# Kernel tuning notes

Hardware: AMD Instinct MI355X
Metric: run time of the kernel (lower is better)

The kernel has to match this reference:

```python
import jax, jax.numpy as jnp
import numpy as np

B, N, F_IN, K, NUM_CLASSES = 16, 2048, 8, 35, 4
EPS = 1e-5


def _bn(x, g, b):
    # BatchNorm in training mode: stats over all leading (batch/node/edge) dims.
    ax = tuple(range(x.ndim - 1))
    mu = jnp.mean(x, axis=ax, keepdims=True)
    var = jnp.var(x, axis=ax, keepdims=True)
    return g * (x - mu) * jax.lax.rsqrt(var + EPS) + b


def _edge_feats(h, k):
    # h: [B,N,C]. Dynamic kNN within each graph (self included, as torch_cluster.knn),
    # then EdgeConv features cat([x_i, x_j - x_i]) -> [B,N,k,2C].
    sq = jnp.sum(h * h, -1)                                   # [B,N]
    d = sq[:, :, None] + sq[:, None, :] - 2.0 * jnp.einsum('bnc,bmc->bnm', h, h)
    _, idx = jax.lax.top_k(-d, k)                             # [B,N,k]
    hj = jax.vmap(lambda hb, ib: hb[ib])(h, idx)              # [B,N,k,C]
    hi = jnp.broadcast_to(h[:, :, None, :], hj.shape)
    return jnp.concatenate([hi, hj - hi], axis=-1)


def _forward(x, w1, b1, g1, bt1, w2, b2, g2, bt2, w3, b3, w4, b4,
             w5, b5, w6, b6, g6, bt6, w7, b7, g7, bt7, w8, b8):
    # conv1: DynamicEdgeConv(MLP([16,64,64,64]), k, 'max'); plain_last => 3rd linear bare
    e = _edge_feats(x, K)                                     # [B,N,K,16]
    h = jax.nn.relu(_bn(e @ w1 + b1, g1, bt1))
    h = jax.nn.relu(_bn(h @ w2 + b2, g2, bt2))
    h = h @ w3 + b3
    x1 = jnp.max(h, axis=2)                                   # [B,N,64] scatter-max over k
    # conv2: DynamicEdgeConv(MLP([128,128]), k, 'max'); single plain linear
    e2 = _edge_feats(x1, K)                                   # [B,N,K,128]
    x2 = jnp.max(e2 @ w4 + b4, axis=2)                        # [B,N,128]
    out = jnp.concatenate([x1, x2], axis=-1) @ w5 + b5        # [B,N,256]
    pooled = jnp.max(out, axis=1)                             # [B,256] global_max_pool
    # head MLP([256,128,64,4], dropout eval-mode, batch_norm), plain_last
    h = jax.nn.relu(_bn(pooled @ w6 + b6, g6, bt6))
    h = jax.nn.relu(_bn(h @ w7 + b7, g7, bt7))
    return h @ w8 + b8                                        # [B,4]


def setup_inputs() -> dict:
    key = jax.random.key(0)
    ks = jax.random.split(key, 12)

    def lin(kk, fi, fo):
        k1, k2 = jax.random.split(kk)
        w = jax.random.normal(k1, (fi, fo), jnp.float32) / np.sqrt(fi).astype(np.float32)
        b = jax.random.normal(k2, (fo,), jnp.float32) * 0.01
        return w, b

    x = jax.random.normal(ks[0], (B, N, F_IN), jnp.float32)
    w1, b1 = lin(ks[1], 2 * F_IN, 64)
    w2, b2 = lin(ks[2], 64, 64)
    w3, b3 = lin(ks[3], 64, 64)
    w4, b4 = lin(ks[4], 2 * 64, 128)
    w5, b5 = lin(ks[5], 128 + 64, 256)
    w6, b6 = lin(ks[6], 256, 128)
    w7, b7 = lin(ks[7], 128, 64)
    w8, b8 = lin(ks[8], 64, NUM_CLASSES)
    ones, zeros = jnp.ones, jnp.zeros
    return {
        'x': x,
        'w1': w1, 'b1': b1, 'g1': ones(64), 'bt1': zeros(64),
        'w2': w2, 'b2': b2, 'g2': ones(64), 'bt2': zeros(64),
        'w3': w3, 'b3': b3,
        'w4': w4, 'b4': b4,
        'w5': w5, 'b5': b5,
        'w6': w6, 'b6': b6, 'g6': ones(128), 'bt6': zeros(128),
        'w7': w7, 'b7': b7, 'g7': ones(64), 'bt7': zeros(64),
        'w8': w8, 'b8': b8,
    }


def reference(x, w1, b1, g1, bt1, w2, b2, g2, bt2, w3, b3, w4, b4,
              w5, b5, w6, b6, g6, bt6, w7, b7, g7, bt7, w8, b8):
    return _forward(x, w1, b1, g1, bt1, w2, b2, g2, bt2, w3, b3, w4, b4,
                    w5, b5, w6, b6, g6, bt6, w7, b7, g7, bt7, w8, b8)
```

## Files before the change

### kernel.cpp

```cpp
#include <hip/hip_runtime.h>
#include <cfloat>
#include <cstdint>

constexpr int Bn   = 16;
constexpr int Nn   = 2048;
constexpr int Fin  = 8;
constexpr int Kn   = 35;
constexpr int NODES = Bn * Nn;
constexpr int EDG   = NODES * Kn;
constexpr int NSTATB = 1024;
constexpr float EPSV = 1e-5f;

typedef _Float16 f16;
typedef _Float16 f16x2 __attribute__((ext_vector_type(2)));

__device__ __forceinline__ unsigned enc_f(float f){
    unsigned u = __float_as_uint(f);
    return (u & 0x80000000u) ? ~u : (u | 0x80000000u);
}
__device__ __forceinline__ float dec_f(unsigned e){
    unsigned u = (e & 0x80000000u) ? (e ^ 0x80000000u) : ~e;
    return __uint_as_float(u);
}

template<int C>
__global__ __launch_bounds__(256) void sq_kernel(const float* __restrict__ h, float* __restrict__ sq){
    int i = blockIdx.x * 256 + threadIdx.x;
    if (i >= NODES) return;
    const float* p = h + (size_t)i * C;
    float s = 0.f;
#pragma unroll
    for (int c = 0; c < C; c++) s += p[c] * p[c];
    sq[i] = s;
}

template<int C>
__global__ __launch_bounds__(256) void knn_kernel(const float* __restrict__ h, const float* __restrict__ sq,
                                                  int* __restrict__ idxout){
    __shared__ float dist[4][Nn];
    __shared__ float hi4[4][C];
    __shared__ float sqi[4];
    __shared__ float statred[4][2][4];
    __shared__ unsigned long long keybuf[4][128];
    int t  = threadIdx.x;
    int b  = blockIdx.x >> 9;
    int i0 = (blockIdx.x & 511) * 4;
    int w  = t >> 6, lane = t & 63;

    for (int i = t; i < 4 * C; i += 256)
        hi4[i / C][i % C] = h[((size_t)(b * Nn) + i0 + i / C) * C + (i % C)];
    if (t < 4) sqi[t] = sq[b * Nn + i0 + t];
    __syncthreads();

    const float4* H0 = (const float4*)hi4[0];
    const float4* H1 = (const float4*)hi4[1];
    const float4* H2 = (const float4*)hi4[2];
    const float4* H3 = (const float4*)hi4[3];
    float ps0=0.f,ps1=0.f,ps2=0.f,ps3=0.f, pq0=0.f,pq1=0.f,pq2=0.f,pq3=0.f;
    for (int j = t; j < Nn; j += 256){
        const float4* hj = (const float4*)(h + ((size_t)(b * Nn) + j) * C);
        float d0 = 0.f, d1 = 0.f, d2 = 0.f, d3 = 0.f;
#pragma unroll 4
        for (int c4 = 0; c4 < C / 4; c4++){
            float4 v = hj[c4];
            float4 a0 = H0[c4], a1 = H1[c4], a2 = H2[c4], a3 = H3[c4];
            d0 += a0.x*v.x + a0.y*v.y + a0.z*v.z + a0.w*v.w;
            d1 += a1.x*v.x + a1.y*v.y + a1.z*v.z + a1.w*v.w;
            d2 += a2.x*v.x + a2.y*v.y + a2.z*v.z + a2.w*v.w;
            d3 += a3.x*v.x + a3.y*v.y + a3.z*v.z + a3.w*v.w;
        }
        float sj = sq[b * Nn + j];
        float D0 = sqi[0] + sj - 2.f*d0; dist[0][j] = D0; ps0 += D0; pq0 += D0*D0;
        float D1 = sqi[1] + sj - 2.f*d1; dist[1][j] = D1; ps1 += D1; pq1 += D1*D1;
        float D2 = sqi[2] + sj - 2.f*d2; dist[2][j] = D2; ps2 += D2; pq2 += D2*D2;
        float D3 = sqi[3] + sj - 2.f*d3; dist[3][j] = D3; ps3 += D3; pq3 += D3*D3;
    }
#pragma unroll
    for (int d = 1; d < 64; d <<= 1){
        ps0 += __shfl_xor(ps0, d); pq0 += __shfl_xor(pq0, d);
        ps1 += __shfl_xor(ps1, d); pq1 += __shfl_xor(pq1, d);
        ps2 += __shfl_xor(ps2, d); pq2 += __shfl_xor(pq2, d);
        ps3 += __shfl_xor(ps3, d); pq3 += __shfl_xor(pq3, d);
    }
    if (lane == 0){
        statred[0][0][w] = ps0; statred[0][1][w] = pq0;
        statred[1][0][w] = ps1; statred[1][1][w] = pq1;
        statred[2][0][w] = ps2; statred[2][1][w] = pq2;
        statred[3][0][w] = ps3; statred[3][1][w] = pq3;
    }
    __syncthreads();

    const float* dw = dist[w];
    float smu = statred[w][0][0] + statred[w][0][1] + statred[w][0][2] + statred[w][0][3];
    float sqq = statred[w][1][0] + statred[w][1][1] + statred[w][1][2] + statred[w][1][3];
    float mu = smu * (1.f / (float)Nn);
    float sg = sqrtf(fmaxf(sqq * (1.f / (float)Nn) - mu * mu, 0.f));

    float lo = mu - 8.f * sg;  int clo = 0;
    float hi = FLT_MAX;        int chi = Nn;

    {
        float PV[5] = { mu - 2.5f*sg, mu - 1.9f*sg, mu - 1.45f*sg, mu - 1.1f*sg, mu };
        int CC[5] = {0,0,0,0,0};
        for (int s8 = 0; s8 < 32; s8 += 8){
            float vv[8];
#pragma unroll
            for (int u = 0; u < 8; u++) vv[u] = dw[(s8 + u) * 64 + lane];
#pragma unroll
            for (int pi = 0; pi < 5; pi++){
                int c = 0;
#pragma unroll
                for (int u = 0; u < 8; u++) c += __popcll(__ballot(vv[u] < PV[pi]));
                CC[pi] += c;
            }
        }
#pragma unroll
        for (int pi = 0; pi < 5; pi++){
            if (CC[pi] >= Kn){ if (PV[pi] < hi){ hi = PV[pi]; chi = CC[pi]; } }
            else             { if (PV[pi] > lo){ lo = PV[pi]; clo = CC[pi]; } }
        }
    }

    for (int it = 0; it < 24 && chi > 128; it++){
        int den = (chi - clo) > 0 ? (chi - clo) : 1;
        float piv = (it & 1) ? 0.5f * (lo + hi)
                             : lo + (hi - lo) * ((float)(96 - clo) / (float)den);
        if (!(piv > lo && piv < hi)) piv = 0.5f * (lo + hi);
        if (!(piv > lo && piv < hi)) break;
        int c = 0;
        for (int s8 = 0; s8 < 32; s8 += 8){
            float vv[8];
#pragma unroll
            for (int u = 0; u < 8; u++) vv[u] = dw[(s8 + u) * 64 + lane];
#pragma unroll
            for (int u = 0; u < 8; u++) c += __popcll(__ballot(vv[u] < piv));
        }
        if (c >= Kn){ hi = piv; chi = c; } else { lo = piv; clo = c; }
    }

    size_t obase = ((size_t)(b * Nn) + i0 + w) * Kn;

    if (chi <= 128){
        keybuf[w][lane]      = ~0ull;
        keybuf[w][lane + 64] = ~0ull;
        unsigned long long me_lower = (1ull << lane) - 1ull;
        int boff = 0;
        for (int s8 = 0; s8 < 32; s8 += 8){
            float vv[8];
#pragma unroll
            for (int u = 0; u < 8; u++) vv[u] = dw[(s8 + u) * 64 + lane];
#pragma unroll
            for (int u = 0; u < 8; u++){
                bool cnd = vv[u] < hi;
                unsigned long long m = __ballot(cnd);
                if (cnd){
                    int o = boff + __popcll(m & me_lower);
                    keybuf[w][o] = (((unsigned long long)enc_f(vv[u])) << 16) | (unsigned)((s8 + u) * 64 + lane);
                }
                boff += __popcll(m);
            }
        }
        unsigned long long k0 = keybuf[w][lane];
        unsigned long long k1 = keybuf[w][lane + 64];
        int r0 = 0, r1 = 0;
        int nR = (chi + 7) & ~7;
        for (int j2 = 0; j2 < nR; j2 += 8){
            unsigned long long a0 = keybuf[w][j2+0], a1 = keybuf[w][j2+1];
            unsigned long long a2 = keybuf[w][j2+2], a3 = keybuf[w][j2+3];
            unsigned long long a4 = keybuf[w][j2+4], a5 = keybuf[w][j2+5];
            unsigned long long a6 = keybuf[w][j2+6], a7 = keybuf[w][j2+7];
            r0 += (a0<k0)+(a1<k0)+(a2<k0)+(a3<k0)+(a4<k0)+(a5<k0)+(a6<k0)+(a7<k0);
            r1 += (a0<k1)+(a1<k1)+(a2<k1)+(a3<k1)+(a4<k1)+(a5<k1)+(a6<k1)+(a7<k1);
        }
        if (lane < chi      && r0 < Kn) idxout[obase + r0] = (int)(k0 & 0xffffu);
        if (lane + 64 < chi && r1 < Kn) idxout[obase + r1] = (int)(k1 & 0xffffu);
    } else {
        unsigned selmask = 0u;
        for (int e = 0; e < Kn; e++){
            unsigned long long best = ~0ull;
#pragma unroll
            for (int s = 0; s < 32; s++){
                float v = dw[s * 64 + lane];
                if (v < hi && !((selmask >> s) & 1)){
                    unsigned long long key = (((unsigned long long)enc_f(v)) << 16) | (unsigned)(s * 64 + lane);
                    best = (key < best) ? key : best;
                }
            }
#pragma unroll
            for (int d = 1; d < 64; d <<= 1){
                unsigned long long ov = __shfl_xor(best, d);
                best = (ov < best) ? ov : best;
            }
            int jj = (int)(best & 0xffffu);
            if ((jj & 63) == lane) selmask |= 1u << (jj >> 6);
            if (lane == 0) idxout[obase + e] = jj;
        }
    }
}

__global__ __launch_bounds__(256) void pre1_kernel(const float* __restrict__ x,
        const float* __restrict__ w1, const float* __restrict__ b1,
        float* __restrict__ p, float* __restrict__ q){
    int t = threadIdx.x, w = t >> 6, c = t & 63;
    float wd[8], wb[8];
#pragma unroll
    for (int f = 0; f < 8; f++){
        float wbv = w1[(8 + f) * 64 + c];
        wb[f] = wbv;
        wd[f] = w1[f * 64 + c] - wbv;
    }
    float b1c = b1[c];
    int slot = blockIdx.x * 4 + w;
    for (int it = 0; it < 16; it++){
        int node = slot + it * 2048;
        const float* xp = x + (size_t)node * Fin;
        float pv = b1c, qv = 0.f;
#pragma unroll
        for (int f = 0; f < 8; f++){
            float xv = xp[f];
            pv += xv * wd[f]; qv += xv * wb[f];
        }
        p[(size_t)node * 64 + c] = pv;
        q[(size_t)node * 64 + c] = qv;
    }
}

__global__ __launch_bounds__(256) void stats1_kernel(const float* __restrict__ p, const float* __restrict__ q,
        const int* __restrict__ idx, float* __restrict__ sumP, float* __restrict__ ssqP){
    __shared__ float red[2][4][64];
    int t = threadIdx.x, w = t >> 6, c = t & 63;
    float s = 0.f, ss = 0.f;
    int slot = blockIdx.x * 4 + w;
    for (int it = 0; it < 8; it++){
        int node = slot + it * 4096;
        int b = node >> 11;
        float pc = p[(size_t)node * 64 + c];
        const int* ip = idx + (size_t)node * Kn;
        for (int k = 0; k < Kn; k++){
            int j = ip[k];
            float z = pc + q[((size_t)(b << 11) + j) * 64 + c];
            s += z; ss += z * z;
        }
    }
    red[0][w][c] = s; red[1][w][c] = ss;
    __syncthreads();
    if (w == 0){
        sumP[blockIdx.x * 64 + c] = red[0][0][c] + red[0][1][c] + red[0][2][c] + red[0][3][c];
        ssqP[blockIdx.x * 64 + c] = red[1][0][c] + red[1][1][c] + red[1][2][c] + red[1][3][c];
    }
}

__global__ void finalize_kernel(const float* __restrict__ sumP, const float* __restrict__ ssqP,
        const float* __restrict__ gg, const float* __restrict__ bt,
        float* __restrict__ scale, float* __restrict__ shift, float inv_count){
    int c = threadIdx.x;
    float s = 0.f, q = 0.f;
    for (int i = 0; i < NSTATB; i++){ s += sumP[i * 64 + c]; q += ssqP[i * 64 + c]; }
    float mu  = s * inv_count;
    float var = q * inv_count - mu * mu;
    float sc  = gg[c] / sqrtf(var + EPSV);
    scale[c] = sc;
    shift[c] = bt[c] - mu * sc;
}

__global__ __launch_bounds__(256) void stats2_kernel(const float* __restrict__ p, const float* __restrict__ q,
        const int* __restrict__ idx,
        const float* __restrict__ sc1v, const float* __restrict__ sh1v,
        const float* __restrict__ w2, const float* __restrict__ b2,
        float* __restrict__ sumP, float* __restrict__ ssqP){
    __shared__ __align__(16) f16 hsh[4][2][64];
    __shared__ float red[2][4][64];
    int t = threadIdx.x, w = t >> 6, c = t & 63;
    f16x2 w2h[32];
#pragma unroll
    for (int f2 = 0; f2 < 32; f2++)
        w2h[f2] = f16x2{(f16)w2[(2*f2)*64 + c], (f16)w2[(2*f2+1)*64 + c]};
    float sc1 = sc1v[c], sh1 = sh1v[c], b2c = b2[c];
    float s = 0.f, ss = 0.f;
    int slot = blockIdx.x * 4 + w;
    for (int it = 0; it < 8; it++){
        int node = slot + it * 4096;
        int b = node >> 11;
        float pc = p[(size_t)node * 64 + c];
        const int* ip = idx + (size_t)node * Kn;
        for (int k = 0; k < Kn; k++){
            int j = ip[k];
            float z = pc + q[((size_t)(b << 11) + j) * 64 + c];
            float h1 = fmaxf(0.f, z * sc1 + sh1);
            hsh[w][k & 1][c] = (f16)h1;
            const uint4* h4 = (const uint4*)hsh[w][k & 1];
            float za0=0.f, za1=0.f, za2=0.f, za3=0.f;
#pragma unroll
            for (int i = 0; i < 8; i++){
                uint4 hv = h4[i];
                za0 = __builtin_amdgcn_fdot2(__builtin_bit_cast(f16x2, hv.x), w2h[4*i+0], za0, false);
                za1 = __builtin_amdgcn_fdot2(__builtin_bit_cast(f16x2, hv.y), w2h[4*i+1], za1, false);
                za2 = __builtin_amdgcn_fdot2(__builtin_bit_cast(f16x2, hv.z), w2h[4*i+2], za2, false);
                za3 = __builtin_amdgcn_fdot2(__builtin_bit_cast(f16x2, hv.w), w2h[4*i+3], za3, false);
            }
            float z2 = b2c + ((za0 + za1) + (za2 + za3));
            s += z2; ss += z2 * z2;
        }
    }
    red[0][w][c] = s; red[1][w][c] = ss;
    __syncthreads();
    if (w == 0){
        sumP[blockIdx.x * 64 + c] = red[0][0][c] + red[0][1][c] + red[0][2][c] + red[0][3][c];
        ssqP[blockIdx.x * 64 + c] = red[1][0][c] + red[1][1][c] + red[1][2][c] + red[1][3][c];
    }
}

__global__ __launch_bounds__(256) void conv1_kernel(const float* __restrict__ p, const float* __restrict__ q,
        const int* __restrict__ idx,
        const float* __restrict__ sc1v, const float* __restrict__ sh1v,
        const float* __restrict__ w2, const float* __restrict__ b2,
        const float* __restrict__ sc2v, const float* __restrict__ sh2v,
        const float* __restrict__ w3, const float* __restrict__ b3,
        float* __restrict__ x1){
    __shared__ __align__(16) f16 hA[4][2][64];
    __shared__ __align__(16) f16 hB[4][2][64];
    int t = threadIdx.x, w = t >> 6, c = t & 63;
    f16x2 w2h[32], w3h[32];
#pragma unroll
    for (int f2 = 0; f2 < 32; f2++){
        w2h[f2] = f16x2{(f16)w2[(2*f2)*64 + c], (f16)w2[(2*f2+1)*64 + c]};
        w3h[f2] = f16x2{(f16)w3[(2*f2)*64 + c], (f16)w3[(2*f2+1)*64 + c]};
    }
    float sc1 = sc1v[c], sh1 = sh1v[c], sc2 = sc2v[c], sh2 = sh2v[c];
    float b2c = b2[c], b3c = b3[c];
    int node = blockIdx.x * 4 + w;
    int b = node >> 11;
    float pc = p[(size_t)node * 64 + c];
    const int* ip = idx + (size_t)node * Kn;
    float acc = -FLT_MAX;
    for (int k = 0; k < Kn; k++){
        int j = ip[k];
        float z = pc + q[((size_t)(b << 11) + j) * 64 + c];
        float h1 = fmaxf(0.f, z * sc1 + sh1);
        hA[w][k & 1][c] = (f16)h1;
        const uint4* h4 = (const uint4*)hA[w][k & 1];
        float za0=0.f, za1=0.f, za2=0.f, za3=0.f;
#pragma unroll
        for (int i = 0; i < 8; i++){
            uint4 hv = h4[i];
            za0 = __builtin_amdgcn_fdot2(__builtin_bit_cast(f16x2, hv.x), w2h[4*i+0], za0, false);
            za1 = __builtin_amdgcn_fdot2(__builtin_bit_cast(f16x2, hv.y), w2h[4*i+1], za1, false);
            za2 = __builtin_amdgcn_fdot2(__builtin_bit_cast(f16x2, hv.z), w2h[4*i+2], za2, false);
            za3 = __builtin_amdgcn_fdot2(__builtin_bit_cast(f16x2, hv.w), w2h[4*i+3], za3, false);
        }
        float z2 = b2c + ((za0 + za1) + (za2 + za3));
        float h2 = fmaxf(0.f, z2 * sc2 + sh2);
        hB[w][k & 1][c] = (f16)h2;
        const uint4* g4 = (const uint4*)hB[w][k & 1];
        float zb0=0.f, zb1=0.f, zb2=0.f, zb3=0.f;
#pragma unroll
        for (int i = 0; i < 8; i++){
            uint4 hv = g4[i];
            zb0 = __builtin_amdgcn_fdot2(__builtin_bit_cast(f16x2, hv.x), w3h[4*i+0], zb0, false);
            zb1 = __builtin_amdgcn_fdot2(__builtin_bit_cast(f16x2, hv.y), w3h[4*i+1], zb1, false);
            zb2 = __builtin_amdgcn_fdot2(__builtin_bit_cast(f16x2, hv.z), w3h[4*i+2], zb2, false);
            zb3 = __builtin_amdgcn_fdot2(__builtin_bit_cast(f16x2, hv.w), w3h[4*i+3], zb3, false);
        }
        float z3 = b3c + ((zb0 + zb1) + (zb2 + zb3));
        acc = fmaxf(acc, z3);
    }
    x1[(size_t)node * 64 + c] = acc;
}

__global__ __launch_bounds__(256) void pre2_kernel(const float* __restrict__ x1,
        const float* __restrict__ w4, const float* __restrict__ b4,
        float* __restrict__ u, float* __restrict__ v){
    __shared__ float x1s[16][64];
    int t = threadIdx.x;
    int c = t & 127, h = t >> 7;
    float wd[64], wb[64];
#pragma unroll
    for (int f = 0; f < 64; f++){
        float wbv = w4[(64 + f) * 128 + c];
        wb[f] = wbv;
        wd[f] = w4[f * 128 + c] - wbv;
    }
    float b4c = b4[c];
    int base = blockIdx.x * 16;
    for (int i = t; i < 16 * 64; i += 256)
        x1s[i >> 6][i & 63] = x1[(size_t)(base + (i >> 6)) * 64 + (i & 63)];
    __syncthreads();
    for (int n = 0; n < 8; n++){
        int node = base + h * 8 + n;
        const float4* xr = (const float4*)x1s[h * 8 + n];
        float u0 = 0.f, u1 = 0.f, v0 = 0.f, v1 = 0.f;
#pragma unroll
        for (int f4 = 0; f4 < 16; f4++){
            float4 xv = xr[f4];
            float pa = xv.x * wd[4*f4] + xv.y * wd[4*f4+1] + xv.z * wd[4*f4+2] + xv.w * wd[4*f4+3];
            float pb = xv.x * wb[4*f4] + xv.y * wb[4*f4+1] + xv.z * wb[4*f4+2] + xv.w * wb[4*f4+3];
            if (f4 & 1){ u1 += pa; v1 += pb; } else { u0 += pa; v0 += pb; }
        }
        u[(size_t)node * 128 + c] = b4c + u0 + u1;
        v[(size_t)node * 128 + c] = v0 + v1;
    }
}

__global__ __launch_bounds__(256) void gmax2_kernel(const float* __restrict__ v, const int* __restrict__ idx,
        float* __restrict__ x2){
    int t = threadIdx.x, g = t >> 7, c = t & 127;
    int node = blockIdx.x * 2 + g;
    int b = node >> 11;
    const int* ip = idx + (size_t)node * Kn;
    float vm = -FLT_MAX;
    for (int k = 0; k < Kn; k++){
        int j = ip[k];
        vm = fmaxf(vm, v[((size_t)(b << 11) + j) * 128 + c]);
    }
    x2[(size_t)node * 128 + c] += vm;
}

__global__ __launch_bounds__(256) void outpool_kernel(const float* __restrict__ x1, const float* __restrict__ x2,
        const float* __restrict__ w5, const float* __restrict__ b5, unsigned* __restrict__ pooled){
    __shared__ float rows[8][192];
    int t = threadIdx.x;
    int node0 = blockIdx.x * 8;
    for (int i = t; i < 8 * 192; i += 256){
        int e = i / 192, f = i - e * 192;
        int nd = node0 + e;
        rows[e][f] = (f < 64) ? x1[(size_t)nd * 64 + f] : x2[(size_t)nd * 128 + f - 64];
    }
    __syncthreads();
    float z[8];
#pragma unroll
    for (int e = 0; e < 8; e++) z[e] = b5[t];
    for (int f = 0; f < 192; f++){
        float w = w5[f * 256 + t];
#pragma unroll
        for (int e = 0; e < 8; e++) z[e] += rows[e][f] * w;
    }
    float m = z[0];
#pragma unroll
    for (int e = 1; e < 8; e++) m = fmaxf(m, z[e]);
    int b = node0 >> 11;
    atomicMax(&pooled[b * 256 + t], enc_f(m));
}

__global__ __launch_bounds__(256) void head_kernel(const unsigned* __restrict__ pooledE,
        const float* __restrict__ w6, const float* __restrict__ b6, const float* __restrict__ g6, const float* __restrict__ bt6,
        const float* __restrict__ w7, const float* __restrict__ b7, const float* __restrict__ g7, const float* __restrict__ bt7,
        const float* __restrict__ w8, const float* __restrict__ b8, float* __restrict__ out){
    __shared__ float P[16][256];
    __shared__ float H6[16][128];
    __shared__ float H7[16][64];
    int t = threadIdx.x;
    for (int i = t; i < 16 * 256; i += 256) P[i >> 8][i & 255] = dec_f(pooledE[i]);
    __syncthreads();
    for (int i = t; i < 16 * 128; i += 256){
        int r = i >> 7, c = i & 127;
        float z = b6[c];
        for (int f = 0; f < 256; f++) z += P[r][f] * w6[f * 128 + c];
        H6[r][c] = z;
    }
    __syncthreads();
    if (t < 128){
        float s = 0.f, q = 0.f;
        for (int r = 0; r < 16; r++){ float v = H6[r][t]; s += v; q += v * v; }
        float mu = s * (1.f / 16.f);
        float var = q * (1.f / 16.f) - mu * mu;
        float sc = g6[t] / sqrtf(var + EPSV);
        float sh = bt6[t] - mu * sc;
        for (int r = 0; r < 16; r++) H6[r][t] = fmaxf(0.f, H6[r][t] * sc + sh);
    }
    __syncthreads();
    for (int i = t; i < 16 * 64; i += 256){
        int r = i >> 6, c = i & 63;
        float z = b7[c];
        for (int f = 0; f < 128; f++) z += H6[r][f] * w7[f * 64 + c];
        H7[r][c] = z;
    }
    __syncthreads();
    if (t < 64){
        float s = 0.f, q = 0.f;
        for (int r = 0; r < 16; r++){ float v = H7[r][t]; s += v; q += v * v; }
        float mu = s * (1.f / 16.f);
        float var = q * (1.f / 16.f) - mu * mu;
        float sc = g7[t] / sqrtf(var + EPSV);
        float sh = bt7[t] - mu * sc;
        for (int r = 0; r < 16; r++) H7[r][t] = fmaxf(0.f, H7[r][t] * sc + sh);
    }
    __syncthreads();
    if (t < 64){
        int r = t >> 2, c = t & 3;
        float z = b8[c];
        for (int f = 0; f < 64; f++) z += H7[r][f] * w8[f * 4 + c];
        out[t] = z;
    }
}

extern "C" void kernel_launch(void* const* d_in, const int* in_sizes, int n_in,
                              void* d_out, int out_size, void* d_ws, size_t ws_size,
                              hipStream_t stream){
    const float* x   = (const float*)d_in[0];
    const float* w1  = (const float*)d_in[1];
    const float* b1  = (const float*)d_in[2];
    const float* g1  = (const float*)d_in[3];
    const float* bt1 = (const float*)d_in[4];
    const float* w2  = (const float*)d_in[5];
    const float* b2  = (const float*)d_in[6];
    const float* g2  = (const float*)d_in[7];
    const float* bt2 = (const float*)d_in[8];
    const float* w3  = (const float*)d_in[9];
    const float* b3  = (const float*)d_in[10];
    const float* w4  = (const float*)d_in[11];
    const float* b4  = (const float*)d_in[12];
    const float* w5  = (const float*)d_in[13];
    const float* b5  = (const float*)d_in[14];
    const float* w6  = (const float*)d_in[15];
    const float* b6  = (const float*)d_in[16];
    const float* g6  = (const float*)d_in[17];
    const float* bt6 = (const float*)d_in[18];
    const float* w7  = (const float*)d_in[19];
    const float* b7  = (const float*)d_in[20];
    const float* g7  = (const float*)d_in[21];
    const float* bt7 = (const float*)d_in[22];
    const float* w8  = (const float*)d_in[23];
    const float* b8  = (const float*)d_in[24];
    float* out = (float*)d_out;

    char* ws = (char*)d_ws;
    size_t off = 0;
    auto alloc = [&](size_t bytes)->char*{
        char* p = ws + off;
        off += (bytes + 255) & ~(size_t)255;
        return p;
    };
    int*      idx1   = (int*)alloc((size_t)EDG * 4);
    int*      idx2   = (int*)alloc((size_t)EDG * 4);
    float*    sq1    = (float*)alloc((size_t)NODES * 4);
    float*    sq2    = (float*)alloc((size_t)NODES * 4);
    float*    x1     = (float*)alloc((size_t)NODES * 64 * 4);
    float*    x2     = (float*)alloc((size_t)NODES * 128 * 4);
    float*    sumP   = (float*)alloc((size_t)NSTATB * 64 * 4);
    float*    ssqP   = (float*)alloc((size_t)NSTATB * 64 * 4);
    float*    scale1 = (float*)alloc(64 * 4);
    float*    shift1 = (float*)alloc(64 * 4);
    float*    scale2 = (float*)alloc(64 * 4);
    float*    shift2 = (float*)alloc(64 * 4);
    unsigned* pooled = (unsigned*)alloc((size_t)Bn * 256 * 4);
    float*    p      = (float*)alloc((size_t)NODES * 64 * 4);
    float*    q      = (float*)alloc((size_t)NODES * 64 * 4);
    float*    v      = p;

    hipMemsetAsync(pooled, 0, (size_t)Bn * 256 * 4, stream);

    sq_kernel<8><<<(NODES + 255) / 256, 256, 0, stream>>>(x, sq1);
    knn_kernel<8><<<NODES / 4, 256, 0, stream>>>(x, sq1, idx1);
    pre1_kernel<<<512, 256, 0, stream>>>(x, w1, b1, p, q);
    stats1_kernel<<<NSTATB, 256, 0, stream>>>(p, q, idx1, sumP, ssqP);
    finalize_kernel<<<1, 64, 0, stream>>>(sumP, ssqP, g1, bt1, scale1, shift1, 1.0f / (float)EDG);
    stats2_kernel<<<NSTATB, 256, 0, stream>>>(p, q, idx1, scale1, shift1, w2, b2, sumP, ssqP);
    finalize_kernel<<<1, 64, 0, stream>>>(sumP, ssqP, g2, bt2, scale2, shift2, 1.0f / (float)EDG);
    conv1_kernel<<<NODES / 4, 256, 0, stream>>>(p, q, idx1, scale1, shift1,
                                                w2, b2, scale2, shift2, w3, b3, x1);
    sq_kernel<64><<<(NODES + 255) / 256, 256, 0, stream>>>(x1, sq2);
    knn_kernel<64><<<NODES / 4, 256, 0, stream>>>(x1, sq2, idx2);
    pre2_kernel<<<NODES / 16, 256, 0, stream>>>(x1, w4, b4, x2, v);
    gmax2_kernel<<<NODES / 2, 256, 0, stream>>>(v, idx2, x2);
    outpool_kernel<<<NODES / 8, 256, 0, stream>>>(x1, x2, w5, b5, pooled);
    head_kernel<<<1, 256, 0, stream>>>(pooled, w6, b6, g6, bt6, w7, b7, g7, bt7, w8, b8, out);
}
```

Before: 1.408 ms.

## Register-block kNN distance loop for C=64 and cache distance row in registers

For the 64-channel kNN pass, each thread now computes four candidate nodes per group and loads the query-row weights once per channel chunk, reusing them across the four candidates. This cuts repeated LDS reads of the query features and exposes more independent global loads. Each wave also copies its 2048-entry distance row into 32 registers once, instead of rereading shared memory in every pivot-count, compaction and selection pass. The cost is much higher register pressure, which could lower occupancy or cause spills.

After: 1.755 ms. +24.6%, slower.

```diff
diff --git a/kernel.cpp b/kernel.cpp
--- a/kernel.cpp
+++ b/kernel.cpp
@@ -57,23 +57,61 @@
     const float4* H2 = (const float4*)hi4[2];
     const float4* H3 = (const float4*)hi4[3];
     float ps0=0.f,ps1=0.f,ps2=0.f,ps3=0.f, pq0=0.f,pq1=0.f,pq2=0.f,pq3=0.f;
-    for (int j = t; j < Nn; j += 256){
-        const float4* hj = (const float4*)(h + ((size_t)(b * Nn) + j) * C);
-        float d0 = 0.f, d1 = 0.f, d2 = 0.f, d3 = 0.f;
-#pragma unroll 4
-        for (int c4 = 0; c4 < C / 4; c4++){
-            float4 v = hj[c4];
-            float4 a0 = H0[c4], a1 = H1[c4], a2 = H2[c4], a3 = H3[c4];
-            d0 += a0.x*v.x + a0.y*v.y + a0.z*v.z + a0.w*v.w;
-            d1 += a1.x*v.x + a1.y*v.y + a1.z*v.z + a1.w*v.w;
-            d2 += a2.x*v.x + a2.y*v.y + a2.z*v.z + a2.w*v.w;
-            d3 += a3.x*v.x + a3.y*v.y + a3.z*v.z + a3.w*v.w;
-        }
-        float sj = sq[b * Nn + j];
-        float D0 = sqi[0] + sj - 2.f*d0; dist[0][j] = D0; ps0 += D0; pq0 += D0*D0;
-        float D1 = sqi[1] + sj - 2.f*d1; dist[1][j] = D1; ps1 += D1; pq1 += D1*D1;
-        float D2 = sqi[2] + sj - 2.f*d2; dist[2][j] = D2; ps2 += D2; pq2 += D2*D2;
-        float D3 = sqi[3] + sj - 2.f*d3; dist[3][j] = D3; ps3 += D3; pq3 += D3*D3;
+
+    if constexpr (C == 64){
+        for (int jg = 0; jg < 2; jg++){
+            float a0[4]={0.f,0.f,0.f,0.f}, a1[4]={0.f,0.f,0.f,0.f};
+            float a2[4]={0.f,0.f,0.f,0.f}, a3[4]={0.f,0.f,0.f,0.f};
+#pragma unroll
+            for (int ch = 0; ch < 8; ch++){
+                float4 W0a = H0[2*ch], W0b = H0[2*ch+1];
+                float4 W1a = H1[2*ch], W1b = H1[2*ch+1];
+                float4 W2a = H2[2*ch], W2b = H2[2*ch+1];
+                float4 W3a = H3[2*ch], W3b = H3[2*ch+1];
+#pragma unroll
+                for (int jj = 0; jj < 4; jj++){
+                    int j = t + (jg * 4 + jj) * 256;
+                    const float4* hj = (const float4*)(h + ((size_t)(b * Nn) + j) * 64 + ch * 8);
+                    float4 va = hj[0], vb = hj[1];
+                    a0[jj] += W0a.x*va.x + W0a.y*va.y + W0a.z*va.z + W0a.w*va.w
+                            + W0b.x*vb.x + W0b.y*vb.y + W0b.z*vb.z + W0b.w*vb.w;
+                    a1[jj] += W1a.x*va.x + W1a.y*va.y + W1a.z*va.z + W1a.w*va.w
+                            + W1b.x*vb.x + W1b.y*vb.y + W1b.z*vb.z + W1b.w*vb.w;
+                    a2[jj] += W2a.x*va.x + W2a.y*va.y + W2a.z*va.z + W2a.w*va.w
+                            + W2b.x*vb.x + W2b.y*vb.y + W2b.z*vb.z + W2b.w*vb.w;
+                    a3[jj] += W3a.x*va.x + W3a.y*va.y + W3a.z*va.z + W3a.w*va.w
+                            + W3b.x*vb.x + W3b.y*vb.y + W3b.z*vb.z + W3b.w*vb.w;
+                }
+            }
+#pragma unroll
+            for (int jj = 0; jj < 4; jj++){
+                int j = t + (jg * 4 + jj) * 256;
+                float sj = sq[b * Nn + j];
+                float D0 = sqi[0] + sj - 2.f*a0[jj]; dist[0][j] = D0; ps0 += D0; pq0 += D0*D0;
+                float D1 = sqi[1] + sj - 2.f*a1[jj]; dist[1][j] = D1; ps1 += D1; pq1 += D1*D1;
+                float D2 = sqi[2] + sj - 2.f*a2[jj]; dist[2][j] = D2; ps2 += D2; pq2 += D2*D2;
+                float D3 = sqi[3] + sj - 2.f*a3[jj]; dist[3][j] = D3; ps3 += D3; pq3 += D3*D3;
+            }
+        }
+    } else {
+        for (int j = t; j < Nn; j += 256){
+            const float4* hj = (const float4*)(h + ((size_t)(b * Nn) + j) * C);
+            float d0 = 0.f, d1 = 0.f, d2 = 0.f, d3 = 0.f;
+#pragma unroll
+            for (int c4 = 0; c4 < C / 4; c4++){
+                float4 v = hj[c4];
+                float4 q0 = H0[c4], q1 = H1[c4], q2 = H2[c4], q3 = H3[c4];
+                d0 += q0.x*v.x + q0.y*v.y + q0.z*v.z + q0.w*v.w;
+                d1 += q1.x*v.x + q1.y*v.y + q1.z*v.z + q1.w*v.w;
+                d2 += q2.x*v.x + q2.y*v.y + q2.z*v.z + q2.w*v.w;
+                d3 += q3.x*v.x + q3.y*v.y + q3.z*v.z + q3.w*v.w;
+            }
+            float sj = sq[b * Nn + j];
+            float D0 = sqi[0] + sj - 2.f*d0; dist[0][j] = D0; ps0 += D0; pq0 += D0*D0;
+            float D1 = sqi[1] + sj - 2.f*d1; dist[1][j] = D1; ps1 += D1; pq1 += D1*D1;
+            float D2 = sqi[2] + sj - 2.f*d2; dist[2][j] = D2; ps2 += D2; pq2 += D2*D2;
+            float D3 = sqi[3] + sj - 2.f*d3; dist[3][j] = D3; ps3 += D3; pq3 += D3*D3;
+        }
     }
 #pragma unroll
     for (int d = 1; d < 64; d <<= 1){
@@ -91,6 +129,10 @@
     __syncthreads();
 
     const float* dw = dist[w];
+    float dv[32];
+#pragma unroll
+    for (int s = 0; s < 32; s++) dv[s] = dw[s * 64 + lane];
+
     float smu = statred[w][0][0] + statred[w][0][1] + statred[w][0][2] + statred[w][0][3];
     float sqq = statred[w][1][0] + statred[w][1][1] + statred[w][1][2] + statred[w][1][3];
     float mu = smu * (1.f / (float)Nn);
@@ -102,17 +144,14 @@
     {
         float PV[5] = { mu - 2.5f*sg, mu - 1.9f*sg, mu - 1.45f*sg, mu - 1.1f*sg, mu };
         int CC[5] = {0,0,0,0,0};
-        for (int s8 = 0; s8 < 32; s8 += 8){
-            float vv[8];
-#pragma unroll
-            for (int u = 0; u < 8; u++) vv[u] = dw[(s8 + u) * 64 + lane];
-#pragma unroll
-            for (int pi = 0; pi < 5; pi++){
-                int c = 0;
-#pragma unroll
-                for (int u = 0; u < 8; u++) c += __popcll(__ballot(vv[u] < PV[pi]));
-                CC[pi] += c;
-            }
+#pragma unroll
+        for (int s = 0; s < 32; s++){
+            float v = dv[s];
+            CC[0] += __popcll(__ballot(v < PV[0]));
+            CC[1] += __popcll(__ballot(v < PV[1]));
+            CC[2] += __popcll(__ballot(v < PV[2]));
+            CC[3] += __popcll(__ballot(v < PV[3]));
+            CC[4] += __popcll(__ballot(v < PV[4]));
         }
 #pragma unroll
         for (int pi = 0; pi < 5; pi++){
@@ -128,13 +167,8 @@
         if (!(piv > lo && piv < hi)) piv = 0.5f * (lo + hi);
         if (!(piv > lo && piv < hi)) break;
         int c = 0;
-        for (int s8 = 0; s8 < 32; s8 += 8){
-            float vv[8];
-#pragma unroll
-            for (int u = 0; u < 8; u++) vv[u] = dw[(s8 + u) * 64 + lane];
-#pragma unroll
-            for (int u = 0; u < 8; u++) c += __popcll(__ballot(vv[u] < piv));
-        }
+#pragma unroll
+        for (int s = 0; s < 32; s++) c += __popcll(__ballot(dv[s] < piv));
         if (c >= Kn){ hi = piv; chi = c; } else { lo = piv; clo = c; }
     }
 
@@ -145,20 +179,15 @@
         keybuf[w][lane + 64] = ~0ull;
         unsigned long long me_lower = (1ull << lane) - 1ull;
         int boff = 0;
-        for (int s8 = 0; s8 < 32; s8 += 8){
-            float vv[8];
-#pragma unroll
-            for (int u = 0; u < 8; u++) vv[u] = dw[(s8 + u) * 64 + lane];
-#pragma unroll
-            for (int u = 0; u < 8; u++){
-                bool cnd = vv[u] < hi;
-                unsigned long long m = __ballot(cnd);
-                if (cnd){
-                    int o = boff + __popcll(m & me_lower);
-                    keybuf[w][o] = (((unsigned long long)enc_f(vv[u])) << 16) | (unsigned)((s8 + u) * 64 + lane);
-                }
-                boff += __popcll(m);
-            }
+#pragma unroll
+        for (int s = 0; s < 32; s++){
+            bool cnd = dv[s] < hi;
+            unsigned long long m = __ballot(cnd);
+            if (cnd){
+                int o = boff + __popcll(m & me_lower);
+                keybuf[w][o] = (((unsigned long long)enc_f(dv[s])) << 16) | (unsigned)(s * 64 + lane);
+            }
+            boff += __popcll(m);
         }
         unsigned long long k0 = keybuf[w][lane];
         unsigned long long k1 = keybuf[w][lane + 64];
@@ -180,7 +209,7 @@
             unsigned long long best = ~0ull;
 #pragma unroll
             for (int s = 0; s < 32; s++){
-                float v = dw[s * 64 + lane];
+                float v = dv[s];
                 if (v < hi && !((selmask >> s) & 1)){
                     unsigned long long key = (((unsigned long long)enc_f(v)) << 16) | (unsigned)(s * 64 + lane);
                     best = (key < best) ? key : best;
```
